# Performance work log

Measured on AMD Instinct MI355X. Metric: run time of the kernel, lower is better.

Reference implementation:

```python
import jax, jax.numpy as jnp
import numpy as np

VOCAB, E, H, P, B, S = 30522, 1024, 1024, 16, 32, 256
HD = H // 2  # per-direction LSTM hidden


def _lstm_dir(xt, Wih, Whh, bih, bhh, reverse):
    # xt: [S,B,in]; PyTorch gate order i,f,g,o
    Hd = Whh.shape[1]
    Bz = xt.shape[1]
    bias = bih + bhh

    def step(carry, xb):
        h, c = carry
        g = xb @ Wih.T + h @ Whh.T + bias
        i, f, gg, o = jnp.split(g, 4, axis=-1)
        c = jax.nn.sigmoid(f) * c + jax.nn.sigmoid(i) * jnp.tanh(gg)
        h = jax.nn.sigmoid(o) * jnp.tanh(c)
        return (h, c), h

    init = (jnp.zeros((Bz, Hd), xt.dtype), jnp.zeros((Bz, Hd), xt.dtype))
    _, hs = jax.lax.scan(step, init, xt, reverse=reverse)
    return hs  # [S,B,Hd], time-ordered


def _bilstm(x, Wih, Whh, bih, bhh):
    # x: [B,S,in]; Wih: [2,4*HD,in] (dir 0 = fwd, dir 1 = bwd)
    xt = jnp.swapaxes(x, 0, 1)
    fw = _lstm_dir(xt, Wih[0], Whh[0], bih[0], bhh[0], False)
    bw = _lstm_dir(xt, Wih[1], Whh[1], bih[1], bhh[1], True)
    return jnp.swapaxes(jnp.concatenate([fw, bw], axis=-1), 0, 1)  # [B,S,2*HD]


def setup_inputs() -> dict:
    key = jax.random.key(0)
    ks = jax.random.split(key, 20)
    sc = 0.05
    inp = {}
    inp["emb"] = jax.random.normal(ks[0], (VOCAB, E), jnp.float32) * sc
    inp["ctx_emb"] = jax.random.normal(ks[1], (VOCAB, E), jnp.float32) * sc
    inp["prompt_emb"] = jax.random.normal(ks[2], (P, E), jnp.float32) * sc
    # LSTM layer 0: input E; layer 1: input 2*HD = H
    inp["Wih0"] = jax.random.normal(ks[3], (2, 4 * HD, E), jnp.float32) * sc
    inp["Whh0"] = jax.random.normal(ks[4], (2, 4 * HD, HD), jnp.float32) * sc
    inp["bih0"] = jax.random.normal(ks[5], (2, 4 * HD), jnp.float32) * sc
    inp["bhh0"] = jax.random.normal(ks[6], (2, 4 * HD), jnp.float32) * sc
    inp["Wih1"] = jax.random.normal(ks[7], (2, 4 * HD, H), jnp.float32) * sc
    inp["Whh1"] = jax.random.normal(ks[8], (2, 4 * HD, HD), jnp.float32) * sc
    inp["bih1"] = jax.random.normal(ks[9], (2, 4 * HD), jnp.float32) * sc
    inp["bhh1"] = jax.random.normal(ks[10], (2, 4 * HD), jnp.float32) * sc
    inp["W1"] = jax.random.normal(ks[11], (H, H), jnp.float32) * sc
    inp["b1"] = jnp.zeros((H,), jnp.float32)
    inp["W2"] = jax.random.normal(ks[12], (E, H), jnp.float32) * sc
    inp["b2"] = jnp.zeros((E,), jnp.float32)
    inp["input_ids"] = jax.random.randint(ks[13], (B, S), 0, VOCAB)
    # distinct, sorted prompt positions per batch row (torch loop assumes valid slots)
    pk = jax.random.split(ks[14], B)
    perms = jax.vmap(lambda k: jax.random.permutation(k, S)[:P])(pk)
    inp["prompt_indexes"] = jnp.sort(perms, axis=1)
    return inp


def reference(emb, ctx_emb, prompt_emb, Wih0, Whh0, bih0, bhh0,
              Wih1, Whh1, bih1, bhh1, W1, b1, W2, b2,
              input_ids, prompt_indexes):
    raw = emb[input_ids]                               # [B,S,E]
    b_idx = jnp.arange(input_ids.shape[0])[:, None]    # [B,1]
    # unique_prompt branch: detached raw + ctx embedding, scatter prompt embeds
    allb = jax.lax.stop_gradient(raw) + ctx_emb[input_ids]
    allb = allb.at[b_idx, prompt_indexes].set(
        jnp.broadcast_to(prompt_emb, (input_ids.shape[0],) + prompt_emb.shape))
    h = _bilstm(allb, Wih0, Whh0, bih0, bhh0)
    h = _bilstm(h, Wih1, Whh1, bih1, bhh1)             # [B,S,H]
    out = jax.nn.relu(h @ W1.T + b1) @ W2.T + b2       # [B,S,E]
    upd = out[b_idx, prompt_indexes] + prompt_emb      # [B,P,E]
    return raw.at[b_idx, prompt_indexes].set(upd)
```

## Files before the change

### kernel.cpp

```cpp
#include <hip/hip_runtime.h>
#include <hip/hip_bf16.h>
#include <math.h>

constexpr int NB  = 32;
constexpr int NS  = 256;
constexpr int NE  = 1024;
constexpr int NH  = 1024;
constexpr int NHD = 512;
constexpr int NG  = 2048;
constexpr int NP  = 16;
constexpr int NBS = NB * NS;
constexpr int GK  = 1024;

constexpr int UPW  = 8;
constexpr int NWGD = NHD / UPW;

constexpr size_t GT_DIR = (size_t)64 * 256 * 1024;

typedef __attribute__((ext_vector_type(8))) short bf16x8;
typedef __attribute__((ext_vector_type(4))) float f32x4;
typedef unsigned short u16;

__device__ __forceinline__ float sigm(float x) { return 1.0f / (1.0f + __expf(-x)); }
__device__ __forceinline__ u16 f2bf(float f) {
    union { float f; unsigned u; } v; v.f = f;
    unsigned r = v.u + 0x7FFF + ((v.u >> 16) & 1);
    return (u16)(r >> 16);
}
__device__ __forceinline__ float bf2f(u16 b) {
    return __uint_as_float((unsigned)b << 16);
}

__global__ void k_zero(int* p) { p[threadIdx.x] = 0; }

__global__ void k_allb(const float* __restrict__ emb, const float* __restrict__ ctx,
                       const float* __restrict__ pemb, const int* __restrict__ ids,
                       const int* __restrict__ pidx, u16* __restrict__ allb) {
    int r = blockIdx.x;
    int b = r >> 8, s = r & 255;
    __shared__ int ppos;
    if (threadIdx.x == 0) {
        int t = -1;
        #pragma unroll
        for (int p = 0; p < NP; ++p)
            if (pidx[b * NP + p] == s) t = p;
        ppos = t;
    }
    __syncthreads();
    int e = threadIdx.x;
    float4 v;
    if (ppos >= 0) {
        v = ((const float4*)(pemb + (size_t)ppos * NE))[e];
    } else {
        int id = ids[r];
        float4 a = ((const float4*)(emb + (size_t)id * NE))[e];
        float4 c = ((const float4*)(ctx + (size_t)id * NE))[e];
        v = make_float4(a.x + c.x, a.y + c.y, a.z + c.z, a.w + c.w);
    }
    ushort4 o;
    o.x = f2bf(v.x); o.y = f2bf(v.y); o.z = f2bf(v.z); o.w = f2bf(v.w);
    *(ushort4*)(allb + ((size_t)(s * NB + b)) * NE + e * 4) = o;
}

__global__ void k_raw(const float* __restrict__ emb, const int* __restrict__ ids,
                      float* __restrict__ out) {
    int r = blockIdx.x;
    int id = ids[r];
    ((float4*)(out + (size_t)r * NE))[threadIdx.x] =
        ((const float4*)(emb + (size_t)id * NE))[threadIdx.x];
}

__global__ void k_wcvt(const float* __restrict__ Wih, const float* __restrict__ bih,
                       const float* __restrict__ bhh, u16* __restrict__ Wbf,
                       float* __restrict__ biasC) {
    int blk = blockIdx.x;
    int d = blk >> 11, np = blk & 2047;
    int rw = (np & 3) * 512 + (np >> 2);
    const float* src = Wih + ((size_t)d * NG + rw) * GK;
    u16* dst = Wbf + ((size_t)d * NG + np) * GK;
    int t = threadIdx.x;
    float4 v = ((const float4*)src)[t];
    ushort4 o;
    o.x = f2bf(v.x); o.y = f2bf(v.y); o.z = f2bf(v.z); o.w = f2bf(v.w);
    ((ushort4*)dst)[t] = o;
    if (t == 0)
        biasC[d * NG + np] = bih[d * NG + rw] + bhh[d * NG + rw];
}

__global__ __launch_bounds__(256) void k_gemm_m(const u16* __restrict__ A0,
                                                const u16* __restrict__ A1,
                                                int astride,
                                                const u16* __restrict__ W,
                                                const float* __restrict__ bc,
                                                float* __restrict__ Gt) {
    __shared__ char At[128 * 128];
    __shared__ char Wt[128 * 128];
    int tid = threadIdx.x;
    int lane = tid & 63, w = tid >> 6;
    int n0 = blockIdx.x * 128, m0 = blockIdx.y * 128;
    int r = tid >> 1, h = tid & 1;

    f32x4 acc[4][4];
    #pragma unroll
    for (int i = 0; i < 4; ++i)
        #pragma unroll
        for (int j = 0; j < 4; ++j) acc[i][j] = (f32x4){0.f, 0.f, 0.f, 0.f};

    unsigned rsw = (unsigned)((r & 7) << 4);
    for (int kt = 0; kt < GK; kt += 64) {
        {
            int k0 = kt + h * 32;
            const u16* asrc = (k0 < 512) ? (A0 + (size_t)(m0 + r) * astride + k0)
                                         : (A1 + (size_t)(m0 + r) * astride + (k0 - 512));
            const u16* wsrc = W + (size_t)(n0 + r) * GK + k0;
            #pragma unroll
            for (int j = 0; j < 4; ++j) {
                uint4 va = *(const uint4*)(asrc + j * 8);
                *(uint4*)(At + r * 128 + (((unsigned)(h * 64 + j * 16)) ^ rsw)) = va;
                uint4 vw = *(const uint4*)(wsrc + j * 8);
                *(uint4*)(Wt + r * 128 + (((unsigned)(h * 64 + j * 16)) ^ rsw)) = vw;
            }
        }
        __syncthreads();
        #pragma unroll
        for (int sub = 0; sub < 2; ++sub) {
            bf16x8 af[4], bfr[4];
            int kbyte = sub * 64 + (lane >> 4) * 16;
            #pragma unroll
            for (int ni = 0; ni < 4; ++ni) {
                int rr = (w & 1) * 64 + ni * 16 + (lane & 15);
                af[ni] = *(const bf16x8*)(Wt + rr * 128 + ((unsigned)kbyte ^ ((unsigned)((rr & 7) << 4))));
            }
            #pragma unroll
            for (int mi = 0; mi < 4; ++mi) {
                int rr = (w >> 1) * 64 + mi * 16 + (lane & 15);
                bfr[mi] = *(const bf16x8*)(At + rr * 128 + ((unsigned)kbyte ^ ((unsigned)((rr & 7) << 4))));
            }
            #pragma unroll
            for (int mi = 0; mi < 4; ++mi)
                #pragma unroll
                for (int ni = 0; ni < 4; ++ni)
                    acc[mi][ni] = __builtin_amdgcn_mfma_f32_16x16x32_bf16(
                        af[ni], bfr[mi], acc[mi][ni], 0, 0, 0);
        }
        __syncthreads();
    }
    #pragma unroll
    for (int mi = 0; mi < 4; ++mi) {
        int mp = m0 + (w >> 1) * 64 + mi * 16 + (lane & 15);
        int t = mp >> 5, b = mp & 31;
        #pragma unroll
        for (int ni = 0; ni < 4; ++ni) {
            int npb = n0 + (w & 1) * 64 + ni * 16 + (lane >> 4) * 4;
            int unit = npb >> 2;
            float4 bv = *(const float4*)(bc + npb);
            f32x4 a = acc[mi][ni];
            float4 o = make_float4(a[0] + bv.x, a[1] + bv.y, a[2] + bv.z, a[3] + bv.w);
            *(float4*)(Gt + ((size_t)((unit >> 3) * NS + t)) * 1024 + b * 32 + (unit & 7) * 4) = o;
        }
    }
}

__global__ __launch_bounds__(256) void k_lstm_f(const float* __restrict__ Gt,
                                                const float* __restrict__ Whh,
                                                u16* __restrict__ hxb,
                                                int* __restrict__ ctr) {
    __shared__ char hlds[NB * NHD * 2];
    int wg = blockIdx.x;
    int d = wg & 1;
    int slice = wg >> 1;
    int n0 = slice * UPW;
    int tid = threadIdx.x;
    int lane = tid & 63;
    int wv = tid >> 6;
    int ublock = wv & 1, bblock = wv >> 1;
    int* ctrd = ctr + d;
    u16* hxd = hxb + (size_t)d * NS * NB * NHD;
    const float* Gd = Gt + (size_t)d * GT_DIR + (size_t)slice * NS * 1024;

    bf16x8 wfrag[16];
    {
        int rloc = lane & 15;
        int usub = rloc >> 2, g = rloc & 3;
        int kb = lane >> 4;
        const float* wrow = Whh + ((size_t)d * NG + g * NHD + n0 + ublock * 4 + usub) * NHD;
        #pragma unroll
        for (int kk = 0; kk < 16; ++kk) {
            const float* p = wrow + kk * 32 + kb * 8;
            float4 x = *(const float4*)p;
            float4 y = *(const float4*)(p + 4);
            bf16x8 wf;
            wf[0] = (short)f2bf(x.x); wf[1] = (short)f2bf(x.y);
            wf[2] = (short)f2bf(x.z); wf[3] = (short)f2bf(x.w);
            wf[4] = (short)f2bf(y.x); wf[5] = (short)f2bf(y.y);
            wf[6] = (short)f2bf(y.z); wf[7] = (short)f2bf(y.w);
            wfrag[kk] = wf;
        }
    }
    int usub_c = lane >> 4;
    int bcol   = bblock * 16 + (lane & 15);
    int unitC  = n0 + ublock * 4 + usub_c;
    int kb     = lane >> 4;
    int c8 = tid & 7, bRow = tid >> 3;

    float creg = 0.f;
    for (int step = 0; step < NS; ++step) {
        int tt = d ? (NS - 1 - step) : step;
        float4 Gv = *(const float4*)(Gd + (size_t)tt * 1024 + bcol * 32 +
                                     (ublock * 4 + usub_c) * 4);
        f32x4 acc = {0.f, 0.f, 0.f, 0.f};
        if (step) {
            int tprev = d ? tt + 1 : tt - 1;
            const u16* srow = hxd + ((size_t)tprev * NB + bRow) * NHD;
            char* dstrow = hlds + bRow * 1024;
            unsigned rsw = (unsigned)((bRow & 7) << 4);
            #pragma unroll
            for (int i = 0; i < 8; ++i) {
                uint4 v = *(const uint4*)(srow + c8 * 64 + i * 8);
                *(uint4*)(dstrow + (((unsigned)(c8 * 128 + i * 16)) ^ rsw)) = v;
            }
            __syncthreads();
            const char* bbase = hlds + bcol * 1024;
            unsigned bsw = (unsigned)((bcol & 7) << 4);
            #pragma unroll
            for (int kk = 0; kk < 16; ++kk) {
                bf16x8 bf = *(const bf16x8*)(bbase + (((unsigned)(kk * 64 + kb * 16)) ^ bsw));
                acc = __builtin_amdgcn_mfma_f32_16x16x32_bf16(wfrag[kk], bf, acc, 0, 0, 0);
            }
            __syncthreads();
        }
        float ig = sigm(acc[0] + Gv.x);
        float fg = sigm(acc[1] + Gv.y);
        float gg = tanhf(acc[2] + Gv.z);
        float og = sigm(acc[3] + Gv.w);
        creg = fg * creg + ig * gg;
        float hv = og * tanhf(creg);
        __hip_atomic_store(hxd + ((size_t)tt * NB + bcol) * NHD + unitC, f2bf(hv),
                           __ATOMIC_RELAXED, __HIP_MEMORY_SCOPE_AGENT);
        asm volatile("s_waitcnt vmcnt(0)" ::: "memory");
        __syncthreads();
        if (tid == 0) {
            __hip_atomic_fetch_add(ctrd, 1, __ATOMIC_RELAXED, __HIP_MEMORY_SCOPE_AGENT);
            int target = NWGD * (step + 1);
            while (__hip_atomic_load(ctrd, __ATOMIC_RELAXED, __HIP_MEMORY_SCOPE_AGENT) < target)
                __builtin_amdgcn_s_sleep(1);
        }
        __syncthreads();
    }
}

__global__ __launch_bounds__(256) void k_mlp1(const u16* __restrict__ hxb,
                                              const int* __restrict__ pidx,
                                              const float* __restrict__ W1,
                                              const float* __restrict__ b1,
                                              float* __restrict__ mid) {
    __shared__ float As[16][65];
    __shared__ float Ws[16][65];
    int tid = threadIdx.x;
    int tx = tid & 15, ty = tid >> 4;
    int n0 = blockIdx.x * 64, m0 = blockIdx.y * 64;
    int lr = tid >> 2;
    int lk = (tid & 3) * 4;
    int m = m0 + lr;
    int bb = m >> 4;
    int s = pidx[m];
    float acc[4][4] = {};
    for (int kt = 0; kt < GK; kt += 16) {
        int k0 = kt + lk;
        int half = k0 >> 9;
        ushort4 av4 = *(const ushort4*)(hxb + (((size_t)(half * NS + s)) * NB + bb) * NHD + (k0 & 511));
        float4 wv = *(const float4*)(W1 + (size_t)(n0 + lr) * GK + k0);
        As[lk + 0][lr] = bf2f(av4.x); As[lk + 1][lr] = bf2f(av4.y);
        As[lk + 2][lr] = bf2f(av4.z); As[lk + 3][lr] = bf2f(av4.w);
        Ws[lk + 0][lr] = wv.x; Ws[lk + 1][lr] = wv.y;
        Ws[lk + 2][lr] = wv.z; Ws[lk + 3][lr] = wv.w;
        __syncthreads();
        #pragma unroll
        for (int kk = 0; kk < 16; ++kk) {
            float a[4], w[4];
            #pragma unroll
            for (int i = 0; i < 4; ++i) a[i] = As[kk][ty * 4 + i];
            #pragma unroll
            for (int j = 0; j < 4; ++j) w[j] = Ws[kk][tx * 4 + j];
            #pragma unroll
            for (int i = 0; i < 4; ++i)
                #pragma unroll
                for (int j = 0; j < 4; ++j) acc[i][j] += a[i] * w[j];
        }
        __syncthreads();
    }
    #pragma unroll
    for (int j = 0; j < 4; ++j) {
        int n = n0 + tx * 4 + j;
        float bias = b1[n];
        #pragma unroll
        for (int i = 0; i < 4; ++i)
            mid[(size_t)(m0 + ty * 4 + i) * 1024 + n] = fmaxf(acc[i][j] + bias, 0.f);
    }
}

__global__ __launch_bounds__(256) void k_mlp2(const float* __restrict__ mid,
                                              const int* __restrict__ pidx,
                                              const float* __restrict__ W2,
                                              const float* __restrict__ b2,
                                              const float* __restrict__ pemb,
                                              float* __restrict__ out) {
    __shared__ float As[16][65];
    __shared__ float Ws[16][65];
    int tid = threadIdx.x;
    int tx = tid & 15, ty = tid >> 4;
    int n0 = blockIdx.x * 64, m0 = blockIdx.y * 64;
    int lr = tid >> 2;
    int lk = (tid & 3) * 4;
    float acc[4][4] = {};
    for (int kt = 0; kt < GK; kt += 16) {
        float4 av = *(const float4*)(mid + (size_t)(m0 + lr) * GK + kt + lk);
        float4 wv = *(const float4*)(W2 + (size_t)(n0 + lr) * GK + kt + lk);
        As[lk + 0][lr] = av.x; As[lk + 1][lr] = av.y;
        As[lk + 2][lr] = av.z; As[lk + 3][lr] = av.w;
        Ws[lk + 0][lr] = wv.x; Ws[lk + 1][lr] = wv.y;
        Ws[lk + 2][lr] = wv.z; Ws[lk + 3][lr] = wv.w;
        __syncthreads();
        #pragma unroll
        for (int kk = 0; kk < 16; ++kk) {
            float a[4], w[4];
            #pragma unroll
            for (int i = 0; i < 4; ++i) a[i] = As[kk][ty * 4 + i];
            #pragma unroll
            for (int j = 0; j < 4; ++j) w[j] = Ws[kk][tx * 4 + j];
            #pragma unroll
            for (int i = 0; i < 4; ++i)
                #pragma unroll
                for (int j = 0; j < 4; ++j) acc[i][j] += a[i] * w[j];
        }
        __syncthreads();
    }
    #pragma unroll
    for (int i = 0; i < 4; ++i) {
        int m = m0 + ty * 4 + i;
        int bb = m >> 4, p = m & 15;
        int s = pidx[m];
        float* orow = out + ((size_t)(bb * NS + s)) * NE;
        const float* prow = pemb + (size_t)p * NE;
        #pragma unroll
        for (int j = 0; j < 4; ++j) {
            int n = n0 + tx * 4 + j;
            orow[n] = acc[i][j] + b2[n] + prow[n];
        }
    }
}

extern "C" void kernel_launch(void* const* d_in, const int* in_sizes, int n_in,
                              void* d_out, int out_size, void* d_ws, size_t ws_size,
                              hipStream_t stream) {
    const float* emb  = (const float*)d_in[0];
    const float* ctx  = (const float*)d_in[1];
    const float* pemb = (const float*)d_in[2];
    const float* Wih0 = (const float*)d_in[3];
    const float* Whh0 = (const float*)d_in[4];
    const float* bih0 = (const float*)d_in[5];
    const float* bhh0 = (const float*)d_in[6];
    const float* Wih1 = (const float*)d_in[7];
    const float* Whh1 = (const float*)d_in[8];
    const float* bih1 = (const float*)d_in[9];
    const float* bhh1 = (const float*)d_in[10];
    const float* W1   = (const float*)d_in[11];
    const float* b1   = (const float*)d_in[12];
    const float* W2   = (const float*)d_in[13];
    const float* b2   = (const float*)d_in[14];
    const int* ids    = (const int*)d_in[15];
    const int* pidx   = (const int*)d_in[16];
    float* out = (float*)d_out;

    char* ws = (char*)d_ws;
    float* Gt    = (float*)ws;
    u16*   allb  = (u16*)(ws + 134217728u);
    u16*   hx    = (u16*)(ws + 150994944u);
    u16*   Wbf   = (u16*)(ws + 167772160u);
    float* biasC = (float*)(ws + 176160768u);
    float* mid   = (float*)(ws + 176177152u);
    int*   ctr   = (int*)(ws + 178274304u);

    k_zero<<<dim3(1), dim3(4), 0, stream>>>(ctr);
    k_allb<<<dim3(NBS), dim3(256), 0, stream>>>(emb, ctx, pemb, ids, pidx, allb);

    k_wcvt<<<dim3(2 * NG), dim3(256), 0, stream>>>(Wih0, bih0, bhh0, Wbf, biasC);
    for (int d = 0; d < 2; ++d)
        k_gemm_m<<<dim3(NG / 128, NBS / 128), dim3(256), 0, stream>>>(
            allb, allb + 512, 1024, Wbf + (size_t)d * NG * GK, biasC + d * NG,
            Gt + (size_t)d * GT_DIR);
    k_lstm_f<<<dim3(2 * NWGD), dim3(256), 0, stream>>>(Gt, Whh0, hx, ctr);

    k_raw<<<dim3(NBS), dim3(256), 0, stream>>>(emb, ids, out);

    k_wcvt<<<dim3(2 * NG), dim3(256), 0, stream>>>(Wih1, bih1, bhh1, Wbf, biasC);
    for (int d = 0; d < 2; ++d)
        k_gemm_m<<<dim3(NG / 128, NBS / 128), dim3(256), 0, stream>>>(
            hx, hx + (size_t)NS * NB * NHD, 512, Wbf + (size_t)d * NG * GK,
            biasC + d * NG, Gt + (size_t)d * GT_DIR);
    k_lstm_f<<<dim3(2 * NWGD), dim3(256), 0, stream>>>(Gt, Whh1, hx, ctr + 2);

    k_mlp1<<<dim3(16, 8), dim3(256), 0, stream>>>(hx, pidx, W1, b1, mid);
    k_mlp2<<<dim3(16, 8), dim3(256), 0, stream>>>(mid, pidx, W2, b2, pemb, out);
}
```

Baseline: 2.557 ms.

## Double units per LSTM workgroup, read h directly, split grid-barrier counters

The persistent LSTM kernel now gives each workgroup 16 hidden units, so half as many workgroups take part in the per-step grid barrier. Each wave now covers both 16-row batch tiles from registers-resident weights. Hidden-state fragments are read straight from global memory instead of being staged through LDS, which removes two block barriers per step. The barrier counter is split into four padded counters so atomic increments are spread out, and the next step's gate preactivations are prefetched. The trade-offs are more global loads per wave and a polling loop that must read four counters.

```diff
diff --git a/kernel.cpp b/kernel.cpp
--- a/kernel.cpp
+++ b/kernel.cpp
@@ -12,10 +12,9 @@
 constexpr int NBS = NB * NS;
 constexpr int GK  = 1024;
 
-constexpr int UPW  = 8;
+constexpr int UPW  = 16;
 constexpr int NWGD = NHD / UPW;
-
-constexpr size_t GT_DIR = (size_t)64 * 256 * 1024;
+constexpr size_t GT_DIR = (size_t)NWGD * 256 * 2048;
 
 typedef __attribute__((ext_vector_type(8))) short bf16x8;
 typedef __attribute__((ext_vector_type(4))) float f32x4;
@@ -156,34 +155,33 @@
             float4 bv = *(const float4*)(bc + npb);
             f32x4 a = acc[mi][ni];
             float4 o = make_float4(a[0] + bv.x, a[1] + bv.y, a[2] + bv.z, a[3] + bv.w);
-            *(float4*)(Gt + ((size_t)((unit >> 3) * NS + t)) * 1024 + b * 32 + (unit & 7) * 4) = o;
-        }
-    }
-}
-
-__global__ __launch_bounds__(256) void k_lstm_f(const float* __restrict__ Gt,
+            *(float4*)(Gt + ((size_t)((unit >> 4) * NS + t)) * 2048 + b * 64 + (unit & 15) * 4) = o;
+        }
+    }
+}
+
+__global__ __launch_bounds__(256) void k_lstm_d(const float* __restrict__ Gt,
                                                 const float* __restrict__ Whh,
                                                 u16* __restrict__ hxb,
                                                 int* __restrict__ ctr) {
-    __shared__ char hlds[NB * NHD * 2];
     int wg = blockIdx.x;
     int d = wg & 1;
     int slice = wg >> 1;
     int n0 = slice * UPW;
     int tid = threadIdx.x;
     int lane = tid & 63;
-    int wv = tid >> 6;
-    int ublock = wv & 1, bblock = wv >> 1;
-    int* ctrd = ctr + d;
+    int w = tid >> 6;
+    int* ctrd  = ctr + d * 64;
+    int* myctr = ctrd + (slice & 3) * 16;
     u16* hxd = hxb + (size_t)d * NS * NB * NHD;
-    const float* Gd = Gt + (size_t)d * GT_DIR + (size_t)slice * NS * 1024;
+    const float* Gd = Gt + (size_t)d * GT_DIR + (size_t)slice * NS * 2048;
 
     bf16x8 wfrag[16];
     {
         int rloc = lane & 15;
         int usub = rloc >> 2, g = rloc & 3;
         int kb = lane >> 4;
-        const float* wrow = Whh + ((size_t)d * NG + g * NHD + n0 + ublock * 4 + usub) * NHD;
+        const float* wrow = Whh + ((size_t)d * NG + g * NHD + n0 + 4 * w + usub) * NHD;
         #pragma unroll
         for (int kk = 0; kk < 16; ++kk) {
             const float* p = wrow + kk * 32 + kb * 8;
@@ -197,53 +195,71 @@
             wfrag[kk] = wf;
         }
     }
-    int usub_c = lane >> 4;
-    int bcol   = bblock * 16 + (lane & 15);
-    int unitC  = n0 + ublock * 4 + usub_c;
-    int kb     = lane >> 4;
-    int c8 = tid & 7, bRow = tid >> 3;
-
-    float creg = 0.f;
+    int uloc  = 4 * w + (lane >> 4);
+    int unitC = n0 + uloc;
+    int bcol0 = lane & 15;
+    int bcol1 = 16 + bcol0;
+    int kb    = lane >> 4;
+
+    float c0 = 0.f, c1 = 0.f;
+    int ttp = d ? (NS - 1) : 0;
+    float4 Gv0 = *(const float4*)(Gd + (size_t)ttp * 2048 + bcol0 * 64 + uloc * 4);
+    float4 Gv1 = *(const float4*)(Gd + (size_t)ttp * 2048 + bcol1 * 64 + uloc * 4);
+
     for (int step = 0; step < NS; ++step) {
         int tt = d ? (NS - 1 - step) : step;
-        float4 Gv = *(const float4*)(Gd + (size_t)tt * 1024 + bcol * 32 +
-                                     (ublock * 4 + usub_c) * 4);
-        f32x4 acc = {0.f, 0.f, 0.f, 0.f};
+        f32x4 acc0 = {0.f, 0.f, 0.f, 0.f};
+        f32x4 acc1 = {0.f, 0.f, 0.f, 0.f};
         if (step) {
             int tprev = d ? tt + 1 : tt - 1;
-            const u16* srow = hxd + ((size_t)tprev * NB + bRow) * NHD;
-            char* dstrow = hlds + bRow * 1024;
-            unsigned rsw = (unsigned)((bRow & 7) << 4);
-            #pragma unroll
-            for (int i = 0; i < 8; ++i) {
-                uint4 v = *(const uint4*)(srow + c8 * 64 + i * 8);
-                *(uint4*)(dstrow + (((unsigned)(c8 * 128 + i * 16)) ^ rsw)) = v;
+            const u16* h0 = hxd + ((size_t)tprev * NB + bcol0) * NHD + kb * 8;
+            const u16* h1 = hxd + ((size_t)tprev * NB + bcol1) * NHD + kb * 8;
+            #pragma unroll
+            for (int kk = 0; kk < 16; ++kk) {
+                bf16x8 b0 = *(const bf16x8*)(h0 + kk * 32);
+                bf16x8 b1 = *(const bf16x8*)(h1 + kk * 32);
+                acc0 = __builtin_amdgcn_mfma_f32_16x16x32_bf16(wfrag[kk], b0, acc0, 0, 0, 0);
+                acc1 = __builtin_amdgcn_mfma_f32_16x16x32_bf16(wfrag[kk], b1, acc1, 0, 0, 0);
             }
-            __syncthreads();
-            const char* bbase = hlds + bcol * 1024;
-            unsigned bsw = (unsigned)((bcol & 7) << 4);
-            #pragma unroll
-            for (int kk = 0; kk < 16; ++kk) {
-                bf16x8 bf = *(const bf16x8*)(bbase + (((unsigned)(kk * 64 + kb * 16)) ^ bsw));
-                acc = __builtin_amdgcn_mfma_f32_16x16x32_bf16(wfrag[kk], bf, acc, 0, 0, 0);
+        }
+        {
+            float ig = sigm(acc0[0] + Gv0.x);
+            float fg = sigm(acc0[1] + Gv0.y);
+            float gg = tanhf(acc0[2] + Gv0.z);
+            float og = sigm(acc0[3] + Gv0.w);
+            c0 = fg * c0 + ig * gg;
+            float hv = og * tanhf(c0);
+            __hip_atomic_store(hxd + ((size_t)tt * NB + bcol0) * NHD + unitC, f2bf(hv),
+                               __ATOMIC_RELAXED, __HIP_MEMORY_SCOPE_AGENT);
+        }
+        {
+            float ig = sigm(acc1[0] + Gv1.x);
+            float fg = sigm(acc1[1] + Gv1.y);
+            float gg = tanhf(acc1[2] + Gv1.z);
+            float og = sigm(acc1[3] + Gv1.w);
+            c1 = fg * c1 + ig * gg;
+            float hv = og * tanhf(c1);
+            __hip_atomic_store(hxd + ((size_t)tt * NB + bcol1) * NHD + unitC, f2bf(hv),
+                               __ATOMIC_RELAXED, __HIP_MEMORY_SCOPE_AGENT);
+        }
+        if (step + 1 < NS) {
+            int ttn = d ? tt - 1 : tt + 1;
+            Gv0 = *(const float4*)(Gd + (size_t)ttn * 2048 + bcol0 * 64 + uloc * 4);
+            Gv1 = *(const float4*)(Gd + (size_t)ttn * 2048 + bcol1 * 64 + uloc * 4);
+        }
+        asm volatile("s_waitcnt vmcnt(0)" ::: "memory");
+        __syncthreads();
+        if (tid == 0) {
+            __hip_atomic_fetch_add(myctr, 1, __ATOMIC_RELAXED, __HIP_MEMORY_SCOPE_AGENT);
+            int target = (NWGD / 4) * (step + 1);
+            for (;;) {
+                int a = __hip_atomic_load(ctrd +  0, __ATOMIC_RELAXED, __HIP_MEMORY_SCOPE_AGENT);
+                int b = __hip_atomic_load(ctrd + 16, __ATOMIC_RELAXED, __HIP_MEMORY_SCOPE_AGENT);
+                int c = __hip_atomic_load(ctrd + 32, __ATOMIC_RELAXED, __HIP_MEMORY_SCOPE_AGENT);
+                int e = __hip_atomic_load(ctrd + 48, __ATOMIC_RELAXED, __HIP_MEMORY_SCOPE_AGENT);
+                if (a >= target && b >= target && c >= target && e >= target) break;
+                __builtin_amdgcn_s_sleep(1);
             }
-            __syncthreads();
-        }
-        float ig = sigm(acc[0] + Gv.x);
-        float fg = sigm(acc[1] + Gv.y);
-        float gg = tanhf(acc[2] + Gv.z);
-        float og = sigm(acc[3] + Gv.w);
-        creg = fg * creg + ig * gg;
-        float hv = og * tanhf(creg);
-        __hip_atomic_store(hxd + ((size_t)tt * NB + bcol) * NHD + unitC, f2bf(hv),
-                           __ATOMIC_RELAXED, __HIP_MEMORY_SCOPE_AGENT);
-        asm volatile("s_waitcnt vmcnt(0)" ::: "memory");
-        __syncthreads();
-        if (tid == 0) {
-            __hip_atomic_fetch_add(ctrd, 1, __ATOMIC_RELAXED, __HIP_MEMORY_SCOPE_AGENT);
-            int target = NWGD * (step + 1);
-            while (__hip_atomic_load(ctrd, __ATOMIC_RELAXED, __HIP_MEMORY_SCOPE_AGENT) < target)
-                __builtin_amdgcn_s_sleep(1);
         }
         __syncthreads();
     }
@@ -277,15 +293,15 @@
         __syncthreads();
         #pragma unroll
         for (int kk = 0; kk < 16; ++kk) {
-            float a[4], w[4];
+            float a[4], wv2[4];
             #pragma unroll
             for (int i = 0; i < 4; ++i) a[i] = As[kk][ty * 4 + i];
             #pragma unroll
-            for (int j = 0; j < 4; ++j) w[j] = Ws[kk][tx * 4 + j];
+            for (int j = 0; j < 4; ++j) wv2[j] = Ws[kk][tx * 4 + j];
             #pragma unroll
             for (int i = 0; i < 4; ++i)
                 #pragma unroll
-                for (int j = 0; j < 4; ++j) acc[i][j] += a[i] * w[j];
+                for (int j = 0; j < 4; ++j) acc[i][j] += a[i] * wv2[j];
         }
         __syncthreads();
     }
@@ -323,15 +339,15 @@
         __syncthreads();
         #pragma unroll
         for (int kk = 0; kk < 16; ++kk) {
-            float a[4], w[4];
+            float a[4], wv2[4];
             #pragma unroll
             for (int i = 0; i < 4; ++i) a[i] = As[kk][ty * 4 + i];
             #pragma unroll
-            for (int j = 0; j < 4; ++j) w[j] = Ws[kk][tx * 4 + j];
+            for (int j = 0; j < 4; ++j) wv2[j] = Ws[kk][tx * 4 + j];
             #pragma unroll
             for (int i = 0; i < 4; ++i)
                 #pragma unroll
-                for (int j = 0; j < 4; ++j) acc[i][j] += a[i] * w[j];
+                for (int j = 0; j < 4; ++j) acc[i][j] += a[i] * wv2[j];
         }
         __syncthreads();
     }
@@ -381,7 +397,7 @@
     float* mid   = (float*)(ws + 176177152u);
     int*   ctr   = (int*)(ws + 178274304u);
 
-    k_zero<<<dim3(1), dim3(4), 0, stream>>>(ctr);
+    k_zero<<<dim3(1), dim3(256), 0, stream>>>(ctr);
     k_allb<<<dim3(NBS), dim3(256), 0, stream>>>(emb, ctx, pemb, ids, pidx, allb);
 
     k_wcvt<<<dim3(2 * NG), dim3(256), 0, stream>>>(Wih0, bih0, bhh0, Wbf, biasC);
@@ -389,7 +405,7 @@
         k_gemm_m<<<dim3(NG / 128, NBS / 128), dim3(256), 0, stream>>>(
             allb, allb + 512, 1024, Wbf + (size_t)d * NG * GK, biasC + d * NG,
             Gt + (size_t)d * GT_DIR);
-    k_lstm_f<<<dim3(2 * NWGD), dim3(256), 0, stream>>>(Gt, Whh0, hx, ctr);
+    k_lstm_d<<<dim3(2 * NWGD), dim3(256), 0, stream>>>(Gt, Whh0, hx, ctr);
 
     k_raw<<<dim3(NBS), dim3(256), 0, stream>>>(emb, ids, out);
 
@@ -398,7 +414,7 @@
         k_gemm_m<<<dim3(NG / 128, NBS / 128), dim3(256), 0, stream>>>(
             hx, hx + (size_t)NS * NB * NHD, 512, Wbf + (size_t)d * NG * GK,
             biasC + d * NG, Gt + (size_t)d * GT_DIR);
-    k_lstm_f<<<dim3(2 * NWGD), dim3(256), 0, stream>>>(Gt, Whh1, hx, ctr + 2);
+    k_lstm_d<<<dim3(2 * NWGD), dim3(256), 0, stream>>>(Gt, Whh1, hx, ctr + 128);
 
     k_mlp1<<<dim3(16, 8), dim3(256), 0, stream>>>(hx, pidx, W1, b1, mid);
     k_mlp2<<<dim3(16, 8), dim3(256), 0, stream>>>(mid, pidx, W2, b2, pemb, out);
```

After: 3.275 ms. 1.28x slower.
